# Performance work log

Hardware: AMD Instinct MI355X
Metric: run time of the kernel (lower is better)

The kernel has to match this reference:

```python
import jax, jax.numpy as jnp
import numpy as np

B, H, W, C = 64, 32, 32, 384          # batch, spatial resolution, channels
NH, WS = 12, 7                        # num_heads, window_size
HD = C // NH                          # head_dim = key_dim (attn_ratio=1)
MLP_H = 4 * C                         # mlp_ratio=4
SCALE = HD ** -0.5
EPS = 1e-5


def _bias_idxs():
    # replicate Attention.__init__ relative-position index construction
    pts = [(i, j) for i in range(WS) for j in range(WS)]
    offs, idxs = {}, []
    for p1 in pts:
        for p2 in pts:
            o = (abs(p1[0] - p2[0]), abs(p1[1] - p2[1]))
            if o not in offs:
                offs[o] = len(offs)
            idxs.append(offs[o])
    return np.array(idxs, dtype=np.int32).reshape(WS * WS, WS * WS), len(offs)


def setup_inputs() -> dict:
    key = jax.random.key(0)
    ks = jax.random.split(key, 8)
    idxs, n_off = _bias_idxs()
    s = lambda k, shape: jax.random.normal(k, shape, jnp.float32) * 0.02
    return {
        'x': jax.random.normal(ks[0], (B, H * W, C), jnp.float32),
        'ln1_g': jnp.ones((C,), jnp.float32), 'ln1_b': jnp.zeros((C,), jnp.float32),
        'qkv_w': s(ks[1], (C, 3 * C)), 'qkv_b': jnp.zeros((3 * C,), jnp.float32),
        'proj_w': s(ks[2], (C, C)), 'proj_b': jnp.zeros((C,), jnp.float32),
        'attn_biases': s(ks[3], (NH, n_off)),
        'conv_w': s(ks[4], (C, 1, 3, 3)),
        'bn_g': jnp.ones((C,), jnp.float32), 'bn_b': jnp.zeros((C,), jnp.float32),
        'bn_m': jnp.zeros((C,), jnp.float32), 'bn_v': jnp.ones((C,), jnp.float32),
        'ln2_g': jnp.ones((C,), jnp.float32), 'ln2_b': jnp.zeros((C,), jnp.float32),
        'fc1_w': s(ks[5], (C, MLP_H)), 'fc1_b': jnp.zeros((MLP_H,), jnp.float32),
        'fc2_w': s(ks[6], (MLP_H, C)), 'fc2_b': jnp.zeros((C,), jnp.float32),
        'bias_idxs': jnp.asarray(idxs),
    }


def _ln(x, g, b):
    m = x.mean(-1, keepdims=True)
    v = ((x - m) ** 2).mean(-1, keepdims=True)
    return (x - m) * jax.lax.rsqrt(v + EPS) * g + b


def _block(x, ln1_g, ln1_b, qkv_w, qkv_b, proj_w, proj_b, attn_biases,
           conv_w, bn_g, bn_b, bn_m, bn_v, ln2_g, ln2_b,
           fc1_w, fc1_b, fc2_w, fc2_b, bias_idxs):
    Bb, L, Cc = x.shape
    res = x
    # ---- window partition with padding ----
    xi = x.reshape(Bb, H, W, Cc)
    pad_b = (WS - H % WS) % WS
    pad_r = (WS - W % WS) % WS
    xi = jnp.pad(xi, ((0, 0), (0, pad_b), (0, pad_r), (0, 0)))
    pH, pW = H + pad_b, W + pad_r
    nHw, nWw = pH // WS, pW // WS
    xw = (xi.reshape(Bb, nHw, WS, nWw, WS, Cc)
            .transpose(0, 1, 3, 2, 4, 5)
            .reshape(Bb * nHw * nWw, WS * WS, Cc))
    # ---- windowed attention with gathered relative-position bias ----
    Bw, N, _ = xw.shape
    xn = _ln(xw, ln1_g, ln1_b)
    qkv = (xn @ qkv_w + qkv_b).reshape(Bw, N, NH, 3 * HD)
    q, k, v = jnp.split(qkv, 3, axis=-1)              # each [Bw, N, NH, HD]
    ab = attn_biases[:, bias_idxs]                     # gather -> [NH, N, N]
    attn = jnp.einsum('bnhd,bmhd->bhnm', q, k) * SCALE + ab
    attn = jax.nn.softmax(attn, axis=-1)
    aw = jnp.einsum('bhnm,bmhd->bnhd', attn, v).reshape(Bw, N, Cc)
    aw = aw @ proj_w + proj_b
    # ---- window merge / unpad ----
    xi = (aw.reshape(Bb, nHw, nWw, WS, WS, Cc)
            .transpose(0, 1, 3, 2, 4, 5)
            .reshape(Bb, pH, pW, Cc))[:, :H, :W]
    x = res + xi.reshape(Bb, L, Cc)
    # ---- depthwise 3x3 conv + BN (eval semantics), NCHW ----
    xc = x.transpose(0, 2, 1).reshape(Bb, Cc, H, W)
    xc = jax.lax.conv_general_dilated(xc, conv_w, (1, 1), ((1, 1), (1, 1)),
                                      feature_group_count=Cc)
    xc = ((xc - bn_m[:, None, None]) * jax.lax.rsqrt(bn_v[:, None, None] + 1e-5)
          * bn_g[:, None, None] + bn_b[:, None, None])
    x = xc.reshape(Bb, Cc, L).transpose(0, 2, 1)
    # ---- MLP (LayerNorm -> fc1 -> GELU -> fc2), residual ----
    h = jax.nn.gelu(_ln(x, ln2_g, ln2_b) @ fc1_w + fc1_b, approximate=False)
    return x + (h @ fc2_w + fc2_b)


def reference(x, ln1_g, ln1_b, qkv_w, qkv_b, proj_w, proj_b, attn_biases,
              conv_w, bn_g, bn_b, bn_m, bn_v, ln2_g, ln2_b,
              fc1_w, fc1_b, fc2_w, fc2_b, bias_idxs):
    return _block(x, ln1_g, ln1_b, qkv_w, qkv_b, proj_w, proj_b, attn_biases,
                  conv_w, bn_g, bn_b, bn_m, bn_v, ln2_g, ln2_b,
                  fc1_w, fc1_b, fc2_w, fc2_b, bias_idxs)
```

## Files before the change

kernel.cpp:

```cpp
#include <hip/hip_runtime.h>
#include <hip/hip_bf16.h>
#include <math.h>

#define NHEAD 12
#define CDIM 384
#define QKVC 1152
#define MLPH 1536
#define SCALE 0.17677669529663687f

typedef __attribute__((ext_vector_type(8))) short short8;
typedef __attribute__((ext_vector_type(4))) float f32x4;

static __device__ __forceinline__ unsigned short f2bf(float f) {
  union { __hip_bfloat16 b; unsigned short u; } c;
  c.b = __float2bfloat16(f);
  return c.u;
}

static __device__ __forceinline__ float gelu_f(float x) {
  float x2 = x * x;
  float t = __builtin_fmaf(0.044715f * x2, x, x);
  float e = __expf(-1.5957691216057308f * t);
  return x / (1.f + e);
}

__global__ void pad_qkv_kernel(const float* __restrict__ lb, const float* __restrict__ Wq,
                               const float* __restrict__ bq, __hip_bfloat16* __restrict__ outp) {
  int j = blockIdx.x * blockDim.x + threadIdx.x;
  if (j >= QKVC) return;
  float s = bq[j];
  for (int c = 0; c < CDIM; c++) s += lb[c] * Wq[(size_t)c * QKVC + j];
  outp[j] = __float2bfloat16(s);
}

__global__ void expand_bias(const float* __restrict__ biases, const int* __restrict__ bidx,
                            float* __restrict__ Bexp, int n_off) {
  int h = blockIdx.x;
  for (int e = threadIdx.x; e < 4096; e += 256) {
    int n = e >> 6, m = e & 63;
    float v;
    if (m >= 49) v = -1e30f;
    else if (n >= 49) v = 0.f;
    else v = biases[h * n_off + bidx[n * 49 + m]];
    Bexp[h * 4096 + e] = v;
  }
}

__global__ void wfragq(const float* __restrict__ W, unsigned short* __restrict__ WF) {
  int f = blockIdx.x;
  int lane = threadIdx.x;
  int kk = f % 12, G = f / 12;
  int n = G * 16 + (lane & 15);
  int k = kk * 32 + (lane >> 4) * 8;
  unsigned short* dst = WF + ((size_t)f * 64 + lane) * 8;
#pragma unroll
  for (int j = 0; j < 8; j++) dst[j] = f2bf(W[(size_t)(k + j) * QKVC + n]);
}

__global__ void wfragp(const float* __restrict__ W, unsigned short* __restrict__ WF) {
  int f = blockIdx.x;
  int lane = threadIdx.x;
  int kk = f % 12, G = f / 12;
  int n = G * 16 + (lane & 15);
  int k = kk * 32 + (lane >> 4) * 8;
  unsigned short* dst = WF + ((size_t)f * 64 + lane) * 8;
#pragma unroll
  for (int j = 0; j < 8; j++) dst[j] = f2bf(W[(size_t)(k + j) * CDIM + n]);
}

__global__ void wfrag1(const float* __restrict__ W, unsigned short* __restrict__ WF) {
  int f = blockIdx.x;
  int lane = threadIdx.x;
  int wn = f & 7, kk = (f >> 3) % 12, ks = f / 96;
  int n = ks * 128 + wn * 16 + (lane & 15);
  int k = kk * 32 + (lane >> 4) * 8;
  unsigned short* dst = WF + ((size_t)f * 64 + lane) * 8;
#pragma unroll
  for (int j = 0; j < 8; j++) dst[j] = f2bf(W[(size_t)(k + j) * MLPH + n]);
}

__global__ void wfrag2(const float* __restrict__ W, unsigned short* __restrict__ WF) {
  int f = blockIdx.x;
  int lane = threadIdx.x;
  int j = f % 3, wn = (f / 3) & 7, kk = (f / 24) & 3, ks = f / 96;
  int n = wn * 48 + j * 16 + (lane & 15);
  int k = ks * 128 + kk * 32 + (lane >> 4) * 8;
  unsigned short* dst = WF + ((size_t)f * 64 + lane) * 8;
#pragma unroll
  for (int jj = 0; jj < 8; jj++) dst[jj] = f2bf(W[(size_t)(k + jj) * CDIM + n]);
}

__global__ __launch_bounds__(512) void ln_qkv(
    const float* __restrict__ X, const float* __restrict__ g, const float* __restrict__ b,
    const unsigned short* __restrict__ WQF, const float* __restrict__ BQ,
    __hip_bfloat16* __restrict__ QKV) {
  __shared__ unsigned short Al[64][388];
  int tid = threadIdx.x;
  int m0 = blockIdx.x * 64;
  int wave = tid >> 6, lane = tid & 63;
  int l15 = lane & 15, l4 = lane >> 4;

#pragma unroll
  for (int r8 = 0; r8 < 8; r8++) {
    int row = wave * 8 + r8;
    const float* xr = X + (size_t)(m0 + row) * CDIM;
    float vals[6];
    float s = 0.f;
#pragma unroll
    for (int i = 0; i < 6; i++) { vals[i] = xr[lane + i * 64]; s += vals[i]; }
#pragma unroll
    for (int o = 32; o > 0; o >>= 1) s += __shfl_xor(s, o);
    float mean = s * (1.f / 384.f);
    float vs = 0.f;
#pragma unroll
    for (int i = 0; i < 6; i++) { float d = vals[i] - mean; vs += d * d; }
#pragma unroll
    for (int o = 32; o > 0; o >>= 1) vs += __shfl_xor(vs, o);
    float rs = rsqrtf(vs * (1.f / 384.f) + 1e-5f);
#pragma unroll
    for (int i = 0; i < 6; i++) {
      int c = lane + i * 64;
      Al[row][c] = f2bf((vals[i] - mean) * rs * g[c] + b[c]);
    }
  }
  __syncthreads();

  for (int rd = 0; rd < 9; rd++) {
    int G = rd * 8 + wave;
    f32x4 acc[4] = {};
    const unsigned short* wb = WQF + (size_t)(G * 12) * 512 + lane * 8;
#pragma unroll
    for (int kk = 0; kk < 12; kk++) {
      short8 bf = *(const short8*)(wb + kk * 512);
#pragma unroll
      for (int i = 0; i < 4; i++) {
        short8 af = *(const short8*)&Al[i * 16 + l15][kk * 32 + l4 * 8];
        acc[i] = __builtin_amdgcn_mfma_f32_16x16x32_bf16(af, bf, acc[i], 0, 0, 0);
      }
    }
    int n = G * 16 + l15;
    float bv = BQ[n];
    __hip_bfloat16* dst = QKV + (size_t)m0 * QKVC + n;
#pragma unroll
    for (int i = 0; i < 4; i++)
#pragma unroll
      for (int r = 0; r < 4; r++)
        dst[(size_t)(i * 16 + l4 * 4 + r) * QKVC] = __float2bfloat16(acc[i][r] + bv);
  }
}

__global__ __launch_bounds__(512) void proj_res(
    const __hip_bfloat16* __restrict__ AW, const unsigned short* __restrict__ WPF,
    const float* __restrict__ BP, const float* __restrict__ X,
    __hip_bfloat16* __restrict__ X1) {
  __shared__ unsigned short Al[64][388];
  int tid = threadIdx.x;
  int m0 = blockIdx.x * 64;
  int wave = tid >> 6, lane = tid & 63;
  int l15 = lane & 15, l4 = lane >> 4;

  {
#pragma unroll
    for (int i = 0; i < 6; i++) {
      int u = tid + i * 512;
      int r = u / 48, col = (u % 48) * 8;
      *(uint4*)&Al[r][col] =
          *(const uint4*)((const unsigned short*)AW + (size_t)(m0 + r) * 384 + col);
    }
  }
  __syncthreads();

  f32x4 acc[4][3] = {};
#pragma unroll
  for (int kk = 0; kk < 12; kk++) {
    short8 af[4];
#pragma unroll
    for (int i = 0; i < 4; i++)
      af[i] = *(const short8*)&Al[i * 16 + l15][kk * 32 + l4 * 8];
#pragma unroll
    for (int j = 0; j < 3; j++) {
      int G = wave * 3 + j;
      short8 bf = *(const short8*)(WPF + (size_t)(G * 12 + kk) * 512 + lane * 8);
#pragma unroll
      for (int i = 0; i < 4; i++)
        acc[i][j] = __builtin_amdgcn_mfma_f32_16x16x32_bf16(af[i], bf, acc[i][j], 0, 0, 0);
    }
  }
#pragma unroll
  for (int j = 0; j < 3; j++) {
    int n = (wave * 3 + j) * 16 + l15;
    float bv = BP[n];
#pragma unroll
    for (int i = 0; i < 4; i++)
#pragma unroll
      for (int r = 0; r < 4; r++) {
        int m = m0 + i * 16 + l4 * 4 + r;
        X1[(size_t)m * 384 + n] =
            __float2bfloat16(acc[i][j][r] + bv + X[(size_t)m * 384 + n]);
      }
  }
}

__global__ __launch_bounds__(512, 4) void mlp_fused(
    const __hip_bfloat16* __restrict__ XN, const unsigned short* __restrict__ W1F,
    const float* __restrict__ B1, const unsigned short* __restrict__ W2F,
    const float* __restrict__ B2, const __hip_bfloat16* __restrict__ X2,
    float* __restrict__ OUT) {
  __shared__ unsigned short XNl[64][388];
  __shared__ unsigned short Hl[64][132];
  int tid = threadIdx.x;
  int m0 = blockIdx.x * 64;
  int wave = tid >> 6, lane = tid & 63;
  int wn = wave;
  int l15 = lane & 15, l4 = lane >> 4;

  {
#pragma unroll
    for (int i = 0; i < 6; i++) {
      int u = tid + i * 512;
      int r = u / 48, col = (u % 48) * 8;
      *(uint4*)&XNl[r][col] =
          *(const uint4*)((const unsigned short*)XN + (size_t)(m0 + r) * 384 + col);
    }
  }

  f32x4 acc[4][3] = {};
  __syncthreads();

  for (int ks = 0; ks < 12; ks++) {
    f32x4 hacc[4] = {};
    const unsigned short* w1fb = W1F + ((size_t)(ks * 96 + wn)) * 512 + lane * 8;
#pragma unroll
    for (int kk = 0; kk < 12; kk++) {
      short8 bf0 = *(const short8*)(w1fb + kk * 4096);
#pragma unroll
      for (int i = 0; i < 4; i++) {
        short8 af = *(const short8*)&XNl[i * 16 + l15][kk * 32 + l4 * 8];
        hacc[i] = __builtin_amdgcn_mfma_f32_16x16x32_bf16(af, bf0, hacc[i], 0, 0, 0);
      }
    }
    float b1v = B1[ks * 128 + wn * 16 + l15];
    __syncthreads();
#pragma unroll
    for (int i = 0; i < 4; i++)
#pragma unroll
      for (int r = 0; r < 4; r++) {
        float c = hacc[i][r] + b1v;
        Hl[i * 16 + l4 * 4 + r][wn * 16 + l15] = f2bf(gelu_f(c));
      }
    __syncthreads();
    const unsigned short* w2fb = W2F + ((size_t)(ks * 96 + wn * 3)) * 512 + lane * 8;
#pragma unroll
    for (int kk = 0; kk < 4; kk++) {
      short8 af2[4];
#pragma unroll
      for (int i = 0; i < 4; i++)
        af2[i] = *(const short8*)&Hl[i * 16 + l15][kk * 32 + l4 * 8];
#pragma unroll
      for (int j = 0; j < 3; j++) {
        short8 bf2 = *(const short8*)(w2fb + kk * 12288 + j * 512);
#pragma unroll
        for (int i = 0; i < 4; i++)
          acc[i][j] = __builtin_amdgcn_mfma_f32_16x16x32_bf16(af2[i], bf2, acc[i][j], 0, 0, 0);
      }
    }
  }
#pragma unroll
  for (int j = 0; j < 3; j++) {
    int n = wn * 48 + j * 16 + l15;
    float bv = B2[n];
#pragma unroll
    for (int i = 0; i < 4; i++)
#pragma unroll
      for (int r = 0; r < 4; r++) {
        int m = m0 + i * 16 + l4 * 4 + r;
        OUT[(size_t)m * 384 + n] =
            acc[i][j][r] + bv + __bfloat162float(X2[(size_t)m * 384 + n]);
      }
  }
}

__global__ __launch_bounds__(64) void attn_mfma(
    const __hip_bfloat16* __restrict__ qkv, const __hip_bfloat16* __restrict__ qkv_pad,
    const float* __restrict__ Bexp, __hip_bfloat16* __restrict__ aw) {
  int h = blockIdx.x % NHEAD;
  int w = blockIdx.x / NHEAD;
  int b = w / 25, wi = w % 25;
  int wh = wi / 5, wv = wi % 5;

  __shared__ unsigned short Q[64][40];
  __shared__ unsigned short K[64][40];
  __shared__ unsigned short Vt[32][72];
  __shared__ unsigned short P[64][72];

  int lane = threadIdx.x;
  int l15 = lane & 15, l4 = lane >> 4;

  {
    int t = lane;
    uint4 z = {0, 0, 0, 0};
    uint4 qv[4], kv[4];
    union { uint4 u[4]; unsigned short s[32]; } vu;
    bool use = t < 49;
    const unsigned short* src = (const unsigned short*)qkv_pad + h * 96;
    if (use) {
      int hh = wh * 7 + t / 7, ww = wv * 7 + t % 7;
      if (hh < 32 && ww < 32)
        src = (const unsigned short*)qkv + (size_t)(b * 1024 + hh * 32 + ww) * QKVC + h * 96;
    }
#pragma unroll
    for (int c = 0; c < 4; c++) {
      qv[c]   = use ? *(const uint4*)(src + c * 8)      : z;
      kv[c]   = use ? *(const uint4*)(src + 32 + c * 8) : z;
      vu.u[c] = use ? *(const uint4*)(src + 64 + c * 8) : z;
    }
#pragma unroll
    for (int c = 0; c < 4; c++) {
      *(uint4*)&Q[t][c * 8] = qv[c];
      *(uint4*)&K[t][c * 8] = kv[c];
    }
#pragma unroll
    for (int d = 0; d < 32; d++) Vt[d][t] = vu.s[d];
  }
  __syncthreads();

  f32x4 acc[4][4] = {};
  {
    short8 aq[4], bk[4];
#pragma unroll
    for (int i = 0; i < 4; i++) aq[i] = *(const short8*)&Q[i * 16 + l15][l4 * 8];
#pragma unroll
    for (int j = 0; j < 4; j++) bk[j] = *(const short8*)&K[j * 16 + l15][l4 * 8];
#pragma unroll
    for (int i = 0; i < 4; i++)
#pragma unroll
      for (int j = 0; j < 4; j++)
        acc[i][j] = __builtin_amdgcn_mfma_f32_16x16x32_bf16(aq[i], bk[j], acc[i][j], 0, 0, 0);
  }

  const float* Bh = Bexp + h * 4096;
  float rinv_[4][4];
#pragma unroll
  for (int i = 0; i < 4; i++) {
    float s[4][4];
#pragma unroll
    for (int j = 0; j < 4; j++)
#pragma unroll
      for (int r = 0; r < 4; r++) {
        int n = i * 16 + l4 * 4 + r, m = j * 16 + l15;
        s[j][r] = acc[i][j][r] * SCALE + Bh[n * 64 + m];
      }
#pragma unroll
    for (int r = 0; r < 4; r++) {
      float mx = fmaxf(fmaxf(s[0][r], s[1][r]), fmaxf(s[2][r], s[3][r]));
#pragma unroll
      for (int o = 1; o < 16; o <<= 1) mx = fmaxf(mx, __shfl_xor(mx, o));
      float p[4], sm = 0.f;
#pragma unroll
      for (int j = 0; j < 4; j++) { p[j] = __expf(s[j][r] - mx); sm += p[j]; }
#pragma unroll
      for (int o = 1; o < 16; o <<= 1) sm += __shfl_xor(sm, o);
      rinv_[i][r] = 1.f / sm;
      int n = i * 16 + l4 * 4 + r;
#pragma unroll
      for (int j = 0; j < 4; j++) P[n][j * 16 + l15] = f2bf(p[j]);
    }
  }
  __syncthreads();

  f32x4 o[4][2] = {};
#pragma unroll
  for (int ks = 0; ks < 2; ks++) {
    short8 pa[4], vb[2];
#pragma unroll
    for (int i = 0; i < 4; i++) pa[i] = *(const short8*)&P[i * 16 + l15][ks * 32 + l4 * 8];
#pragma unroll
    for (int j = 0; j < 2; j++) vb[j] = *(const short8*)&Vt[j * 16 + l15][ks * 32 + l4 * 8];
#pragma unroll
    for (int i = 0; i < 4; i++)
#pragma unroll
      for (int j = 0; j < 2; j++)
        o[i][j] = __builtin_amdgcn_mfma_f32_16x16x32_bf16(pa[i], vb[j], o[i][j], 0, 0, 0);
  }

#pragma unroll
  for (int i = 0; i < 4; i++)
#pragma unroll
    for (int r = 0; r < 4; r++) {
      int n = i * 16 + l4 * 4 + r;
      if (n < 49) {
        int hh = wh * 7 + n / 7, ww = wv * 7 + n % 7;
        if (hh < 32 && ww < 32) {
          __hip_bfloat16* dst = aw + (size_t)(b * 1024 + hh * 32 + ww) * CDIM + h * 32;
          float ri = rinv_[i][r];
#pragma unroll
          for (int j = 0; j < 2; j++)
            dst[j * 16 + l15] = __float2bfloat16(o[i][j][r] * ri);
        }
      }
    }
}

__global__ __launch_bounds__(384) void conv_bn_ln_kernel(
    const __hip_bfloat16* __restrict__ X, const float* __restrict__ W9,
    const float* __restrict__ g, const float* __restrict__ bb,
    const float* __restrict__ mm, const float* __restrict__ vv,
    const float* __restrict__ lg, const float* __restrict__ lb,
    __hip_bfloat16* __restrict__ X2, __hip_bfloat16* __restrict__ XN) {
  int nwg = gridDim.x;
  int id = blockIdx.x;
  int nid = (id & 7) * (nwg >> 3) + (id >> 3);
  int yh = nid & 1;
  int x = (nid >> 1) & 31;
  int b = nid >> 6;
  int c = threadIdx.x;

  float w[9];
#pragma unroll
  for (int i = 0; i < 9; i++) w[i] = W9[c * 9 + i];
  float bnsc = rsqrtf(vv[c] + 1e-5f) * g[c];
  float bnsh = bb[c] - mm[c] * bnsc;
  float lgc = lg[c], lbc = lb[c];

  bool xm = x > 0, xp = x < 31;
  const __hip_bfloat16* colbase = X + ((size_t)(b * 1024 + x)) * CDIM + c;

  __shared__ float part[2][6][2];
  int wv = threadIdx.x >> 6, ln = threadIdx.x & 63;

  float w0[3], w1[3], w2[3];
  int y0 = yh * 16;
  if (y0 == 0) {
    w0[0] = w0[1] = w0[2] = 0.f;
  } else {
    const __hip_bfloat16* p = colbase + (size_t)(y0 - 1) * 32 * CDIM;
    w0[0] = xm ? __bfloat162float(p[-CDIM]) : 0.f;
    w0[1] = __bfloat162float(p[0]);
    w0[2] = xp ? __bfloat162float(p[CDIM]) : 0.f;
  }
  {
    const __hip_bfloat16* p = colbase + (size_t)y0 * 32 * CDIM;
    w1[0] = xm ? __bfloat162float(p[-CDIM]) : 0.f;
    w1[1] = __bfloat162float(p[0]);
    w1[2] = xp ? __bfloat162float(p[CDIM]) : 0.f;
  }

  for (int y = y0; y < y0 + 16; y++) {
    if (y + 1 < 32) {
      const __hip_bfloat16* p = colbase + (size_t)(y + 1) * 32 * CDIM;
      w2[0] = xm ? __bfloat162float(p[-CDIM]) : 0.f;
      w2[1] = __bfloat162float(p[0]);
      w2[2] = xp ? __bfloat162float(p[CDIM]) : 0.f;
    } else {
      w2[0] = w2[1] = w2[2] = 0.f;
    }
    float acc = w0[0] * w[0] + w0[1] * w[1] + w0[2] * w[2]
              + w1[0] * w[3] + w1[1] * w[4] + w1[2] * w[5]
              + w2[0] * w[6] + w2[1] * w[7] + w2[2] * w[8];
    float r = acc * bnsc + bnsh;
    size_t tok = (size_t)(b * 1024 + y * 32 + x);
    X2[tok * CDIM + c] = __float2bfloat16(r);

    float s1 = r, s2 = r * r;
#pragma unroll
    for (int o = 32; o > 0; o >>= 1) { s1 += __shfl_xor(s1, o); s2 += __shfl_xor(s2, o); }
    int pb = y & 1;
    if (ln == 0) { part[pb][wv][0] = s1; part[pb][wv][1] = s2; }
    __syncthreads();
    float ts1 = 0.f, ts2 = 0.f;
#pragma unroll
    for (int i = 0; i < 6; i++) { ts1 += part[pb][i][0]; ts2 += part[pb][i][1]; }
    float mean = ts1 * (1.f / 384.f);
    float var = ts2 * (1.f / 384.f) - mean * mean;
    float rstd = rsqrtf(var + 1e-5f);
    XN[tok * CDIM + c] = __float2bfloat16((r - mean) * rstd * lgc + lbc);

    w0[0] = w1[0]; w0[1] = w1[1]; w0[2] = w1[2];
    w1[0] = w2[0]; w1[1] = w2[1]; w1[2] = w2[2];
  }
}

extern "C" void kernel_launch(void* const* d_in, const int* in_sizes, int n_in,
                              void* d_out, int out_size, void* d_ws, size_t ws_size,
                              hipStream_t stream) {
  const float* x      = (const float*)d_in[0];
  const float* ln1_g  = (const float*)d_in[1];
  const float* ln1_b  = (const float*)d_in[2];
  const float* qkv_w  = (const float*)d_in[3];
  const float* qkv_b  = (const float*)d_in[4];
  const float* proj_w = (const float*)d_in[5];
  const float* proj_b = (const float*)d_in[6];
  const float* att_b  = (const float*)d_in[7];
  const float* conv_w = (const float*)d_in[8];
  const float* bn_g   = (const float*)d_in[9];
  const float* bn_b   = (const float*)d_in[10];
  const float* bn_m   = (const float*)d_in[11];
  const float* bn_v   = (const float*)d_in[12];
  const float* ln2_g  = (const float*)d_in[13];
  const float* ln2_b  = (const float*)d_in[14];
  const float* fc1_w  = (const float*)d_in[15];
  const float* fc1_b  = (const float*)d_in[16];
  const float* fc2_w  = (const float*)d_in[17];
  const float* fc2_b  = (const float*)d_in[18];
  const int* bias_idxs = (const int*)d_in[19];
  int n_off = in_sizes[7] / NHEAD;
  float* out = (float*)d_out;

  char* ws = (char*)d_ws;
  size_t off = 0;
  __hip_bfloat16* qkv_pad = (__hip_bfloat16*)(ws + off); off += QKVC * 2;
  off = (off + 255) & ~(size_t)255;
  float* Bexp = (float*)(ws + off); off += (size_t)NHEAD * 4096 * 4;
  unsigned short* wqf = (unsigned short*)(ws + off); off += (size_t)QKVC * CDIM * 2;
  unsigned short* wpf = (unsigned short*)(ws + off); off += (size_t)CDIM * CDIM * 2;
  unsigned short* w1f = (unsigned short*)(ws + off); off += (size_t)MLPH * CDIM * 2;
  unsigned short* w2f = (unsigned short*)(ws + off); off += (size_t)CDIM * MLPH * 2;
  size_t HDR = (off + 255) & ~(size_t)255;

  const size_t PER_TOK = 4608;
  int Bc = 64;
  while (Bc > 1 && HDR + (size_t)Bc * 1024 * PER_TOK > ws_size) Bc >>= 1;
  size_t Tc = (size_t)Bc * 1024;

  off = HDR;
  __hip_bfloat16* xn = (__hip_bfloat16*)(ws + off); off += Tc * CDIM * 2;
  __hip_bfloat16* qkv = (__hip_bfloat16*)(ws + off); off += Tc * QKVC * 2;
  __hip_bfloat16* x1 = qkv;
  __hip_bfloat16* awb = (__hip_bfloat16*)(ws + off); off += Tc * CDIM * 2;
  __hip_bfloat16* x2 = (__hip_bfloat16*)(ws + off); off += Tc * CDIM * 2;

  pad_qkv_kernel<<<dim3(5), dim3(256), 0, stream>>>(ln1_b, qkv_w, qkv_b, qkv_pad);
  expand_bias<<<dim3(NHEAD), dim3(256), 0, stream>>>(att_b, bias_idxs, Bexp, n_off);
  wfragq<<<dim3(864), dim3(64), 0, stream>>>(qkv_w, wqf);
  wfragp<<<dim3(288), dim3(64), 0, stream>>>(proj_w, wpf);
  wfrag1<<<dim3(1152), dim3(64), 0, stream>>>(fc1_w, w1f);
  wfrag2<<<dim3(1152), dim3(64), 0, stream>>>(fc2_w, w2f);

  for (int b0 = 0; b0 < 64; b0 += Bc) {
    const float* xa = x + (size_t)b0 * 1024 * CDIM;
    float* outa = out + (size_t)b0 * 1024 * CDIM;
    int M = (int)Tc;

    ln_qkv<<<dim3(M / 64), dim3(512), 0, stream>>>(xa, ln1_g, ln1_b, wqf, qkv_b, qkv);
    attn_mfma<<<dim3(Bc * 25 * NHEAD), dim3(64), 0, stream>>>(qkv, qkv_pad, Bexp, awb);
    proj_res<<<dim3(M / 64), dim3(512), 0, stream>>>(awb, wpf, proj_b, xa, x1);
    conv_bn_ln_kernel<<<dim3(Bc * 64), dim3(384), 0, stream>>>(
        x1, conv_w, bn_g, bn_b, bn_m, bn_v, ln2_g, ln2_b, x2, xn);
    mlp_fused<<<dim3(M / 64), dim3(512), 0, stream>>>(
        xn, w1f, fc1_b, w2f, fc2_b, x2, outa);
  }
}
```

Before: 759.9 us.

## Double-buffer fc1 weight fragments in registers across MLP hidden chunks

Preloads the next hidden chunk's fc1 weight fragments into a second register set (wA/wB ping-pong) while the current chunk's MFMAs run, unrolling the chunk loop by two. This hides global-load latency for W1 behind compute. The extra 24 short8 registers per lane push register pressure up, so launch bounds drop from 4 to 2 blocks per CU, lowering occupancy. The last iteration issues a redundant prefetch of chunk 0.

```diff
diff --git a/kernel.cpp b/kernel.cpp
--- a/kernel.cpp
+++ b/kernel.cpp
@@ -201,7 +201,7 @@
   }
 }
 
-__global__ __launch_bounds__(512, 4) void mlp_fused(
+__global__ __launch_bounds__(512, 2) void mlp_fused(
     const __hip_bfloat16* __restrict__ XN, const unsigned short* __restrict__ W1F,
     const float* __restrict__ B1, const unsigned short* __restrict__ W2F,
     const float* __restrict__ B2, const __hip_bfloat16* __restrict__ X2,
@@ -225,43 +225,92 @@
   }
 
   f32x4 acc[4][3] = {};
+  const unsigned short* w1b0 = W1F + (size_t)wn * 512 + lane * 8;
+  short8 wA[12], wB[12];
+#pragma unroll
+  for (int kk = 0; kk < 12; kk++)
+    wA[kk] = *(const short8*)(w1b0 + kk * 4096);
+
   __syncthreads();
 
-  for (int ks = 0; ks < 12; ks++) {
-    f32x4 hacc[4] = {};
-    const unsigned short* w1fb = W1F + ((size_t)(ks * 96 + wn)) * 512 + lane * 8;
-#pragma unroll
-    for (int kk = 0; kk < 12; kk++) {
-      short8 bf0 = *(const short8*)(w1fb + kk * 4096);
-#pragma unroll
-      for (int i = 0; i < 4; i++) {
-        short8 af = *(const short8*)&XNl[i * 16 + l15][kk * 32 + l4 * 8];
-        hacc[i] = __builtin_amdgcn_mfma_f32_16x16x32_bf16(af, bf0, hacc[i], 0, 0, 0);
+  for (int S = 0; S < 6; S++) {
+    {
+      const int ks = 2 * S;
+#pragma unroll
+      for (int kk = 0; kk < 12; kk++)
+        wB[kk] = *(const short8*)(w1b0 + (size_t)(ks + 1) * 49152 + kk * 4096);
+      f32x4 hacc[4] = {};
+#pragma unroll
+      for (int kk = 0; kk < 12; kk++)
+#pragma unroll
+        for (int i = 0; i < 4; i++) {
+          short8 af = *(const short8*)&XNl[i * 16 + l15][kk * 32 + l4 * 8];
+          hacc[i] = __builtin_amdgcn_mfma_f32_16x16x32_bf16(af, wA[kk], hacc[i], 0, 0, 0);
+        }
+      float b1v = B1[ks * 128 + wn * 16 + l15];
+      __syncthreads();
+#pragma unroll
+      for (int i = 0; i < 4; i++)
+#pragma unroll
+        for (int r = 0; r < 4; r++) {
+          float c = hacc[i][r] + b1v;
+          Hl[i * 16 + l4 * 4 + r][wn * 16 + l15] = f2bf(gelu_f(c));
+        }
+      __syncthreads();
+      const unsigned short* w2fb = W2F + ((size_t)(ks * 96 + wn * 3)) * 512 + lane * 8;
+#pragma unroll
+      for (int kk = 0; kk < 4; kk++) {
+        short8 af2[4];
+#pragma unroll
+        for (int i = 0; i < 4; i++)
+          af2[i] = *(const short8*)&Hl[i * 16 + l15][kk * 32 + l4 * 8];
+#pragma unroll
+        for (int j = 0; j < 3; j++) {
+          short8 bf2 = *(const short8*)(w2fb + kk * 12288 + j * 512);
+#pragma unroll
+          for (int i = 0; i < 4; i++)
+            acc[i][j] = __builtin_amdgcn_mfma_f32_16x16x32_bf16(af2[i], bf2, acc[i][j], 0, 0, 0);
+        }
       }
     }
-    float b1v = B1[ks * 128 + wn * 16 + l15];
-    __syncthreads();
-#pragma unroll
-    for (int i = 0; i < 4; i++)
-#pragma unroll
-      for (int r = 0; r < 4; r++) {
-        float c = hacc[i][r] + b1v;
-        Hl[i * 16 + l4 * 4 + r][wn * 16 + l15] = f2bf(gelu_f(c));
-      }
-    __syncthreads();
-    const unsigned short* w2fb = W2F + ((size_t)(ks * 96 + wn * 3)) * 512 + lane * 8;
-#pragma unroll
-    for (int kk = 0; kk < 4; kk++) {
-      short8 af2[4];
+    {
+      const int ks = 2 * S + 1;
+      const int ksn = (ks + 1 < 12) ? (ks + 1) : 0;
+#pragma unroll
+      for (int kk = 0; kk < 12; kk++)
+        wA[kk] = *(const short8*)(w1b0 + (size_t)ksn * 49152 + kk * 4096);
+      f32x4 hacc[4] = {};
+#pragma unroll
+      for (int kk = 0; kk < 12; kk++)
+#pragma unroll
+        for (int i = 0; i < 4; i++) {
+          short8 af = *(const short8*)&XNl[i * 16 + l15][kk * 32 + l4 * 8];
+          hacc[i] = __builtin_amdgcn_mfma_f32_16x16x32_bf16(af, wB[kk], hacc[i], 0, 0, 0);
+        }
+      float b1v = B1[ks * 128 + wn * 16 + l15];
+      __syncthreads();
 #pragma unroll
       for (int i = 0; i < 4; i++)
-        af2[i] = *(const short8*)&Hl[i * 16 + l15][kk * 32 + l4 * 8];
-#pragma unroll
-      for (int j = 0; j < 3; j++) {
-        short8 bf2 = *(const short8*)(w2fb + kk * 12288 + j * 512);
+#pragma unroll
+        for (int r = 0; r < 4; r++) {
+          float c = hacc[i][r] + b1v;
+          Hl[i * 16 + l4 * 4 + r][wn * 16 + l15] = f2bf(gelu_f(c));
+        }
+      __syncthreads();
+      const unsigned short* w2fb = W2F + ((size_t)(ks * 96 + wn * 3)) * 512 + lane * 8;
+#pragma unroll
+      for (int kk = 0; kk < 4; kk++) {
+        short8 af2[4];
 #pragma unroll
         for (int i = 0; i < 4; i++)
-          acc[i][j] = __builtin_amdgcn_mfma_f32_16x16x32_bf16(af2[i], bf2, acc[i][j], 0, 0, 0);
+          af2[i] = *(const short8*)&Hl[i * 16 + l15][kk * 32 + l4 * 8];
+#pragma unroll
+        for (int j = 0; j < 3; j++) {
+          short8 bf2 = *(const short8*)(w2fb + kk * 12288 + j * 512);
+#pragma unroll
+          for (int i = 0; i < 4; i++)
+            acc[i][j] = __builtin_amdgcn_mfma_f32_16x16x32_bf16(af2[i], bf2, acc[i][j], 0, 0, 0);
+        }
       }
     }
   }
```

Measured after the change: 731.7 us, median of 2. 1.04x faster.
